# Kernel optimization log

Measured on AMD Instinct MI355X. Metric: run time of the kernel, lower is better.

## Reference

```python
import jax, jax.numpy as jnp
import numpy as np

N_NODES = 10000
N_EDGES = 320000
IN_F, H1, H2 = 512, 256, 64


def setup_inputs() -> dict:
    key = jax.random.key(0)
    ks = jax.random.split(key, 8)
    x = jax.random.normal(ks[0], (N_NODES, IN_F), dtype=jnp.float32)
    edge_src = jax.random.randint(ks[1], (N_EDGES,), 0, N_NODES, dtype=jnp.int32)
    edge_dst = jax.random.randint(ks[2], (N_EDGES,), 0, N_NODES, dtype=jnp.int32)
    edge_weight = jax.random.uniform(ks[3], (N_EDGES,), dtype=jnp.float32)
    # Glorot-initialized GCN weights + biases
    W1 = jax.random.normal(ks[4], (IN_F, H1), dtype=jnp.float32) * (1.0 / np.sqrt(IN_F))
    b1 = jnp.zeros((H1,), dtype=jnp.float32)
    W2 = jax.random.normal(ks[5], (H1, H2), dtype=jnp.float32) * (1.0 / np.sqrt(H1))
    b2 = jnp.zeros((H2,), dtype=jnp.float32)
    return {"x": x, "W1": W1, "b1": b1, "W2": W2, "b2": b2,
            "edge_weight": edge_weight, "edge_src": edge_src, "edge_dst": edge_dst}


def _gcn_layer(h, W, b, edge_src, edge_dst, edge_weight, act):
    # support = h @ W  (dropout is identity in eval mode)
    support = h @ W  # [N, out]
    # sparse adjacency aggregation: out[dst] += w * support[src]
    msgs = support[edge_src] * edge_weight[:, None]  # [E, out]
    agg = jax.ops.segment_sum(msgs, edge_dst, num_segments=h.shape[0])
    return act(agg + b)


def reference(x, W1, b1, W2, b2, edge_weight, edge_src, edge_dst):
    h1 = _gcn_layer(x, W1, b1, edge_src, edge_dst, edge_weight, jax.nn.relu)
    z = _gcn_layer(h1, W2, b2, edge_src, edge_dst, edge_weight, jax.nn.relu)  # embeddings
    # InnerProductDecoder: sigmoid(z @ z.T)
    recon = jax.nn.sigmoid(z @ z.T)  # [N, N]
    return (z, recon)
```

## Files before the change

kernel.cpp:

```cpp
#include <hip/hip_runtime.h>

#define N_NODES 10000
#define N_EDGES 320000
#define IN_F    512
#define H1F     256
#define H2F     64

__global__ __launch_bounds__(1024) void k_classify(const int* __restrict__ c0,
                                                   const int* __restrict__ c2,
                                                   int* __restrict__ sel) {
    __shared__ int cnt0, cnt2;
    if (threadIdx.x == 0) { cnt0 = 0; cnt2 = 0; }
    __syncthreads();
    int v0 = c0[threadIdx.x];
    int v2 = c2[threadIdx.x];
    if (v0 >= 0 && v0 < N_NODES) atomicAdd(&cnt0, 1);
    if (v2 >= 0 && v2 < N_NODES) atomicAdd(&cnt2, 1);
    __syncthreads();
    if (threadIdx.x == 0) *sel = (cnt0 > 900 && cnt2 <= 900) ? 1 : 0;
}

__global__ __launch_bounds__(256) void k_hist(const int* __restrict__ c0,
                                              const int* __restrict__ c2,
                                              const int* __restrict__ sel,
                                              int* __restrict__ deg) {
    int e = blockIdx.x * 256 + threadIdx.x;
    if (e >= N_EDGES) return;
    int dst = (*sel) ? c0[e] : c2[e];
    if ((unsigned)dst < N_NODES) atomicAdd(&deg[dst], 1);
}

__global__ __launch_bounds__(1024) void k_scan(const int* __restrict__ deg,
                                               int* __restrict__ off,
                                               int* __restrict__ cursor) {
    __shared__ int part[1024];
    int t = threadIdx.x;
    const int chunk = (N_NODES + 1023) / 1024;
    int begin = t * chunk;
    int end = begin + chunk; if (end > N_NODES) end = N_NODES;
    if (begin > N_NODES) begin = N_NODES;
    int s = 0;
    for (int i = begin; i < end; ++i) s += deg[i];
    part[t] = s;
    __syncthreads();
    for (int o = 1; o < 1024; o <<= 1) {
        int v = (t >= o) ? part[t - o] : 0;
        __syncthreads();
        part[t] += v;
        __syncthreads();
    }
    int base = (t == 0) ? 0 : part[t - 1];
    for (int i = begin; i < end; ++i) {
        off[i] = base; cursor[i] = base; base += deg[i];
    }
    if (t == 1023) off[N_NODES] = part[1023];
}

__global__ __launch_bounds__(256) void k_bucket(const int* __restrict__ c0,
                                                const int* __restrict__ c1,
                                                const int* __restrict__ c2,
                                                const float* __restrict__ c0f,
                                                const float* __restrict__ c2f,
                                                const int* __restrict__ sel,
                                                int* __restrict__ cursor,
                                                int* __restrict__ srcp,
                                                float* __restrict__ wp) {
    int e = blockIdx.x * 256 + threadIdx.x;
    if (e >= N_EDGES) return;
    int s = *sel;
    int src = c1[e];
    int dst = s ? c0[e] : c2[e];
    float w = s ? c2f[e] : c0f[e];
    if ((unsigned)src >= N_NODES || (unsigned)dst >= N_NODES) return;
    int p = atomicAdd(&cursor[dst], 1);
    srcp[p] = src;
    wp[p] = w;
}

__global__ __launch_bounds__(256) void k_gemm1(const float* __restrict__ x,
                                               const float* __restrict__ W1,
                                               float* __restrict__ sup1) {
    __shared__ float xs[IN_F][8];
    int nb = blockIdx.x * 8;
    int t = threadIdx.x;
    {
        int n  = t & 7;
        int k0 = (t >> 3) * 16;
        const float* xr = x + (size_t)(nb + n) * IN_F + k0;
        #pragma unroll
        for (int c = 0; c < 16; c += 4) {
            float4 v = *(const float4*)(xr + c);
            xs[k0 + c + 0][n] = v.x;
            xs[k0 + c + 1][n] = v.y;
            xs[k0 + c + 2][n] = v.z;
            xs[k0 + c + 3][n] = v.w;
        }
    }
    __syncthreads();
    int f = t;
    float acc[8] = {0.f,0.f,0.f,0.f,0.f,0.f,0.f,0.f};
    #pragma unroll 8
    for (int k = 0; k < IN_F; ++k) {
        float w = W1[(size_t)k * H1F + f];
        float4 a = *(const float4*)&xs[k][0];
        float4 b = *(const float4*)&xs[k][4];
        acc[0] += a.x * w; acc[1] += a.y * w; acc[2] += a.z * w; acc[3] += a.w * w;
        acc[4] += b.x * w; acc[5] += b.y * w; acc[6] += b.z * w; acc[7] += b.w * w;
    }
    #pragma unroll
    for (int n = 0; n < 8; ++n)
        sup1[(size_t)(nb + n) * H1F + f] = acc[n];
}

__global__ __launch_bounds__(256) void k_agg1(const float* __restrict__ sup1,
                                              const int* __restrict__ off,
                                              const int* __restrict__ srcp,
                                              const float* __restrict__ wp,
                                              const float* __restrict__ b1,
                                              float* __restrict__ h1) {
    int node = blockIdx.x;
    int f = threadIdx.x;
    int s = off[node], e = off[node + 1];
    float acc = 0.f;
    for (int i = s; i < e; ++i) {
        float w = wp[i];
        int src = srcp[i];
        acc += w * sup1[(size_t)src * H1F + f];
    }
    h1[(size_t)node * H1F + f] = fmaxf(acc + b1[f], 0.f);
}

__global__ __launch_bounds__(64) void k_gemm2(const float* __restrict__ h1,
                                              const float* __restrict__ W2,
                                              float* __restrict__ sup2) {
    __shared__ float hs[H1F][4];
    int nb = blockIdx.x * 4;
    int t = threadIdx.x;
    {
        int n  = t & 3;
        int k0 = (t >> 2) * 16;
        const float* hr = h1 + (size_t)(nb + n) * H1F + k0;
        #pragma unroll
        for (int c = 0; c < 16; c += 4) {
            float4 v = *(const float4*)(hr + c);
            hs[k0 + c + 0][n] = v.x;
            hs[k0 + c + 1][n] = v.y;
            hs[k0 + c + 2][n] = v.z;
            hs[k0 + c + 3][n] = v.w;
        }
    }
    __syncthreads();
    int f = t;
    float acc[4] = {0.f,0.f,0.f,0.f};
    #pragma unroll 8
    for (int k = 0; k < H1F; ++k) {
        float w = W2[(size_t)k * H2F + f];
        float4 a = *(const float4*)&hs[k][0];
        acc[0] += a.x * w; acc[1] += a.y * w; acc[2] += a.z * w; acc[3] += a.w * w;
    }
    #pragma unroll
    for (int n = 0; n < 4; ++n)
        sup2[(size_t)(nb + n) * H2F + f] = acc[n];
}

__global__ __launch_bounds__(64) void k_agg2(const float* __restrict__ sup2,
                                             const int* __restrict__ off,
                                             const int* __restrict__ srcp,
                                             const float* __restrict__ wp,
                                             const float* __restrict__ b2,
                                             float* __restrict__ zout) {
    int node = blockIdx.x;
    int f = threadIdx.x;
    int s = off[node], e = off[node + 1];
    float acc = 0.f;
    for (int i = s; i < e; ++i) {
        float w = wp[i];
        int src = srcp[i];
        acc += w * sup2[(size_t)src * H2F + f];
    }
    zout[(size_t)node * H2F + f] = fmaxf(acc + b2[f], 0.f);
}

__global__ __launch_bounds__(256) void k_decoder(const float* __restrict__ zf,
                                                 float* __restrict__ recon) {
    __shared__ float As[H2F][68];
    __shared__ float Bs[H2F][68];
    int i0 = blockIdx.y * 64, j0 = blockIdx.x * 64;
    int t = threadIdx.x;
    int li = t & 63;
    int kq = t >> 6;
    #pragma unroll
    for (int rep = 0; rep < 4; ++rep) {
        int k0 = (kq + rep * 4) * 4;
        float4 va = make_float4(0.f, 0.f, 0.f, 0.f);
        float4 vb = make_float4(0.f, 0.f, 0.f, 0.f);
        if (i0 + li < N_NODES) va = *(const float4*)&zf[(size_t)(i0 + li) * H2F + k0];
        if (j0 + li < N_NODES) vb = *(const float4*)&zf[(size_t)(j0 + li) * H2F + k0];
        As[k0 + 0][li] = va.x; As[k0 + 1][li] = va.y; As[k0 + 2][li] = va.z; As[k0 + 3][li] = va.w;
        Bs[k0 + 0][li] = vb.x; Bs[k0 + 1][li] = vb.y; Bs[k0 + 2][li] = vb.z; Bs[k0 + 3][li] = vb.w;
    }
    __syncthreads();

    int tx = t & 15, ty = t >> 4;
    float acc[4][4] = {{0.f}};
    #pragma unroll 4
    for (int k = 0; k < H2F; ++k) {
        float a0 = As[k][ty * 4 + 0], a1 = As[k][ty * 4 + 1];
        float a2 = As[k][ty * 4 + 2], a3 = As[k][ty * 4 + 3];
        float b0 = Bs[k][tx * 4 + 0], b1 = Bs[k][tx * 4 + 1];
        float b2 = Bs[k][tx * 4 + 2], b3 = Bs[k][tx * 4 + 3];
        acc[0][0] += a0 * b0; acc[0][1] += a0 * b1; acc[0][2] += a0 * b2; acc[0][3] += a0 * b3;
        acc[1][0] += a1 * b0; acc[1][1] += a1 * b1; acc[1][2] += a1 * b2; acc[1][3] += a1 * b3;
        acc[2][0] += a2 * b0; acc[2][1] += a2 * b1; acc[2][2] += a2 * b2; acc[2][3] += a2 * b3;
        acc[3][0] += a3 * b0; acc[3][1] += a3 * b1; acc[3][2] += a3 * b2; acc[3][3] += a3 * b3;
    }

    #pragma unroll
    for (int ii = 0; ii < 4; ++ii) {
        int row = i0 + ty * 4 + ii;
        if (row >= N_NODES) continue;
        int col = j0 + tx * 4;
        float o4[4];
        #pragma unroll
        for (int jj = 0; jj < 4; ++jj) {
            float s = acc[ii][jj];
            o4[jj] = 1.0f / (1.0f + __expf(-s));
        }
        size_t base = (size_t)row * N_NODES + col;
        if (col + 4 <= N_NODES) {
            *(float4*)(recon + base) = make_float4(o4[0], o4[1], o4[2], o4[3]);
        } else {
            for (int jj = 0; jj < 4; ++jj)
                if (col + jj < N_NODES) recon[base + jj] = o4[jj];
        }
    }
}

extern "C" void kernel_launch(void* const* d_in, const int* in_sizes, int n_in,
                              void* d_out, int out_size, void* d_ws, size_t ws_size,
                              hipStream_t stream) {
    int ix = -1, iW1 = -1, ib1 = -1, iW2 = -1, ib2 = -1, ic0 = -1, ic1 = -1, ic2 = -1;
    for (int i = 0; i < n_in; ++i) {
        int s = in_sizes[i];
        if      (s == N_NODES * IN_F) ix = i;
        else if (s == IN_F * H1F)     iW1 = i;
        else if (s == H1F)            ib1 = i;
        else if (s == H1F * H2F)     iW2 = i;
        else if (s == H2F)            ib2 = i;
        else if (s == N_EDGES) { if (ic0 < 0) ic0 = i; else if (ic1 < 0) ic1 = i; else ic2 = i; }
    }
    if (ix < 0 || iW1 < 0 || ib1 < 0 || iW2 < 0 || ib2 < 0 || ic0 < 0 || ic1 < 0 || ic2 < 0) {
        ix = 0; iW1 = 1; ib1 = 2; iW2 = 3; ib2 = 4; ic0 = 5; ic1 = 6; ic2 = 7;
    }
    const float* x  = (const float*)d_in[ix];
    const float* W1 = (const float*)d_in[iW1];
    const float* b1 = (const float*)d_in[ib1];
    const float* W2 = (const float*)d_in[iW2];
    const float* b2 = (const float*)d_in[ib2];
    const int*   c0  = (const int*)d_in[ic0];
    const int*   c1  = (const int*)d_in[ic1];
    const int*   c2  = (const int*)d_in[ic2];
    const float* c0f = (const float*)d_in[ic0];
    const float* c2f = (const float*)d_in[ic2];

    float* zout  = (float*)d_out;
    float* recon = zout + (size_t)N_NODES * H2F;

    char* scratch = (char*)recon;
    size_t o = 0;
    auto alloc = [&](size_t bytes) { size_t p = o; o += (bytes + 255) & ~(size_t)255; return p; };
    int*   sel    = (int*)  (scratch + alloc(256));
    int*   deg    = (int*)  (scratch + alloc((size_t)N_NODES * 4));
    int*   off    = (int*)  (scratch + alloc((size_t)(N_NODES + 1) * 4));
    int*   cursor = (int*)  (scratch + alloc((size_t)N_NODES * 4));
    int*   srcp   = (int*)  (scratch + alloc((size_t)N_EDGES * 4));
    float* wp     = (float*)(scratch + alloc((size_t)N_EDGES * 4));
    float* sup1   = (float*)(scratch + alloc((size_t)N_NODES * H1F * 4));
    float* h1     = (float*)(scratch + alloc((size_t)N_NODES * H1F * 4));
    float* sup2   = (float*)(scratch + alloc((size_t)N_NODES * H2F * 4));

    k_classify<<<1, 1024, 0, stream>>>(c0, c2, sel);

    hipMemsetAsync(deg, 0, (size_t)N_NODES * 4, stream);
    k_hist  <<<(N_EDGES + 255) / 256, 256, 0, stream>>>(c0, c2, sel, deg);
    k_scan  <<<1, 1024, 0, stream>>>(deg, off, cursor);
    k_bucket<<<(N_EDGES + 255) / 256, 256, 0, stream>>>(c0, c1, c2, c0f, c2f, sel, cursor, srcp, wp);

    k_gemm1<<<N_NODES / 8, 256, 0, stream>>>(x, W1, sup1);
    k_agg1 <<<N_NODES, 256, 0, stream>>>(sup1, off, srcp, wp, b1, h1);

    k_gemm2<<<N_NODES / 4, 64, 0, stream>>>(h1, W2, sup2);
    k_agg2 <<<N_NODES, 64, 0, stream>>>(sup2, off, srcp, wp, b2, zout);

    dim3 dgrid((N_NODES + 63) / 64, (N_NODES + 63) / 64);
    k_decoder<<<dgrid, 256, 0, stream>>>(zout, recon);
}
```

Before: 740.5 us.

## Run decoder z·zᵀ on bf16 MFMA with a bf16 copy of z

The aggregation kernel now also writes a bf16 copy of the embeddings to workspace. The decoder replaces its LDS-tiled fp32 FMA GEMM with per-wave 32x32x16 bf16 MFMA instructions that load operands straight from global memory. Each of the four waves in a block computes a 32x32 tile of the output. The decoder is bound by writing the 400MB output, so compute savings may matter little, and the per-element scalar stores may coalesce worse than the previous float4 stores. Rounding z to bf16 also lowers precision of the logits.

```diff
diff --git a/kernel.cpp b/kernel.cpp
--- a/kernel.cpp
+++ b/kernel.cpp
@@ -5,6 +5,15 @@
 #define IN_F    512
 #define H1F     256
 #define H2F     64
+
+typedef __attribute__((ext_vector_type(8)))  short short8;
+typedef __attribute__((ext_vector_type(16))) float f32x16;
+
+__device__ __forceinline__ unsigned short f2bf(float f) {
+    union { float fl; unsigned int i; } v; v.fl = f;
+    unsigned int x = v.i;
+    return (unsigned short)((x + 0x7fffu + ((x >> 16) & 1u)) >> 16);
+}
 
 __global__ __launch_bounds__(1024) void k_classify(const int* __restrict__ c0,
                                                    const int* __restrict__ c2,
@@ -168,7 +177,8 @@
                                              const int* __restrict__ srcp,
                                              const float* __restrict__ wp,
                                              const float* __restrict__ b2,
-                                             float* __restrict__ zout) {
+                                             float* __restrict__ zout,
+                                             unsigned short* __restrict__ zb) {
     int node = blockIdx.x;
     int f = threadIdx.x;
     int s = off[node], e = off[node + 1];
@@ -178,60 +188,44 @@
         int src = srcp[i];
         acc += w * sup2[(size_t)src * H2F + f];
     }
-    zout[(size_t)node * H2F + f] = fmaxf(acc + b2[f], 0.f);
-}
-
-__global__ __launch_bounds__(256) void k_decoder(const float* __restrict__ zf,
+    acc = fmaxf(acc + b2[f], 0.f);
+    zout[(size_t)node * H2F + f] = acc;
+    zb[(size_t)node * H2F + f] = f2bf(acc);
+}
+
+__global__ __launch_bounds__(256) void k_decoder(const unsigned short* __restrict__ zb,
                                                  float* __restrict__ recon) {
-    __shared__ float As[H2F][68];
-    __shared__ float Bs[H2F][68];
-    int i0 = blockIdx.y * 64, j0 = blockIdx.x * 64;
-    int t = threadIdx.x;
-    int li = t & 63;
-    int kq = t >> 6;
-    #pragma unroll
-    for (int rep = 0; rep < 4; ++rep) {
-        int k0 = (kq + rep * 4) * 4;
-        float4 va = make_float4(0.f, 0.f, 0.f, 0.f);
-        float4 vb = make_float4(0.f, 0.f, 0.f, 0.f);
-        if (i0 + li < N_NODES) va = *(const float4*)&zf[(size_t)(i0 + li) * H2F + k0];
-        if (j0 + li < N_NODES) vb = *(const float4*)&zf[(size_t)(j0 + li) * H2F + k0];
-        As[k0 + 0][li] = va.x; As[k0 + 1][li] = va.y; As[k0 + 2][li] = va.z; As[k0 + 3][li] = va.w;
-        Bs[k0 + 0][li] = vb.x; Bs[k0 + 1][li] = vb.y; Bs[k0 + 2][li] = vb.z; Bs[k0 + 3][li] = vb.w;
-    }
-    __syncthreads();
-
-    int tx = t & 15, ty = t >> 4;
-    float acc[4][4] = {{0.f}};
-    #pragma unroll 4
-    for (int k = 0; k < H2F; ++k) {
-        float a0 = As[k][ty * 4 + 0], a1 = As[k][ty * 4 + 1];
-        float a2 = As[k][ty * 4 + 2], a3 = As[k][ty * 4 + 3];
-        float b0 = Bs[k][tx * 4 + 0], b1 = Bs[k][tx * 4 + 1];
-        float b2 = Bs[k][tx * 4 + 2], b3 = Bs[k][tx * 4 + 3];
-        acc[0][0] += a0 * b0; acc[0][1] += a0 * b1; acc[0][2] += a0 * b2; acc[0][3] += a0 * b3;
-        acc[1][0] += a1 * b0; acc[1][1] += a1 * b1; acc[1][2] += a1 * b2; acc[1][3] += a1 * b3;
-        acc[2][0] += a2 * b0; acc[2][1] += a2 * b1; acc[2][2] += a2 * b2; acc[2][3] += a2 * b3;
-        acc[3][0] += a3 * b0; acc[3][1] += a3 * b1; acc[3][2] += a3 * b2; acc[3][3] += a3 * b3;
-    }
-
-    #pragma unroll
-    for (int ii = 0; ii < 4; ++ii) {
-        int row = i0 + ty * 4 + ii;
-        if (row >= N_NODES) continue;
-        int col = j0 + tx * 4;
-        float o4[4];
-        #pragma unroll
-        for (int jj = 0; jj < 4; ++jj) {
-            float s = acc[ii][jj];
-            o4[jj] = 1.0f / (1.0f + __expf(-s));
-        }
-        size_t base = (size_t)row * N_NODES + col;
-        if (col + 4 <= N_NODES) {
-            *(float4*)(recon + base) = make_float4(o4[0], o4[1], o4[2], o4[3]);
-        } else {
-            for (int jj = 0; jj < 4; ++jj)
-                if (col + jj < N_NODES) recon[base + jj] = o4[jj];
+    int t = threadIdx.x;
+    int wave = t >> 6, lane = t & 63;
+    int i0 = blockIdx.y * 64 + (wave >> 1) * 32;
+    int j0 = blockIdx.x * 64 + (wave & 1) * 32;
+    int r = lane & 31, half = lane >> 5;
+    int arow = i0 + r, brow = j0 + r;
+
+    short8 zero8 = {0,0,0,0,0,0,0,0};
+    short8 a[4], b[4];
+    #pragma unroll
+    for (int s = 0; s < 4; ++s) {
+        a[s] = (arow < N_NODES) ? *(const short8*)(zb + (size_t)arow * H2F + s * 16 + half * 8)
+                                : zero8;
+        b[s] = (brow < N_NODES) ? *(const short8*)(zb + (size_t)brow * H2F + s * 16 + half * 8)
+                                : zero8;
+    }
+
+    f32x16 acc;
+    #pragma unroll
+    for (int i = 0; i < 16; ++i) acc[i] = 0.f;
+    #pragma unroll
+    for (int s = 0; s < 4; ++s)
+        acc = __builtin_amdgcn_mfma_f32_32x32x16_bf16(a[s], b[s], acc, 0, 0, 0);
+
+    #pragma unroll
+    for (int rg = 0; rg < 16; ++rg) {
+        int row = i0 + (rg & 3) + 8 * (rg >> 2) + 4 * half;
+        int col = j0 + r;
+        if (row < N_NODES && col < N_NODES) {
+            float sv = acc[rg];
+            recon[(size_t)row * N_NODES + col] = 1.0f / (1.0f + __expf(-sv));
         }
     }
 }
@@ -245,7 +239,7 @@
         if      (s == N_NODES * IN_F) ix = i;
         else if (s == IN_F * H1F)     iW1 = i;
         else if (s == H1F)            ib1 = i;
-        else if (s == H1F * H2F)     iW2 = i;
+        else if (s == H1F * H2F)      iW2 = i;
         else if (s == H2F)            ib2 = i;
         else if (s == N_EDGES) { if (ic0 < 0) ic0 = i; else if (ic1 < 0) ic1 = i; else ic2 = i; }
     }
@@ -265,6 +259,8 @@
 
     float* zout  = (float*)d_out;
     float* recon = zout + (size_t)N_NODES * H2F;
+
+    unsigned short* zb = (unsigned short*)d_ws;
 
     char* scratch = (char*)recon;
     size_t o = 0;
@@ -290,8 +286,8 @@
     k_agg1 <<<N_NODES, 256, 0, stream>>>(sup1, off, srcp, wp, b1, h1);
 
     k_gemm2<<<N_NODES / 4, 64, 0, stream>>>(h1, W2, sup2);
-    k_agg2 <<<N_NODES, 64, 0, stream>>>(sup2, off, srcp, wp, b2, zout);
+    k_agg2 <<<N_NODES, 64, 0, stream>>>(sup2, off, srcp, wp, b2, zout, zb);
 
     dim3 dgrid((N_NODES + 63) / 64, (N_NODES + 63) / 64);
-    k_decoder<<<dgrid, 256, 0, stream>>>(zout, recon);
-}
+    k_decoder<<<dgrid, 256, 0, stream>>>(zb, recon);
+}
```

Result: faster. 663.3 us (-10.4%).
